# Performance work log

Measured on AMD Instinct MI355X. Metric: run time of the kernel, lower is better.

The kernel has to match this reference:

```python
import jax, jax.numpy as jnp
import numpy as np

N_NODES = 100000
N_EDGES = 1600000
IN_FEATS = 256
HEADS = 4
OUT_FEATS = 32


def setup_inputs() -> dict:
    key = jax.random.key(0)
    k1, k2, k3, k4, k5, k6 = jax.random.split(key, 6)
    feat = jax.random.normal(k1, (N_NODES, IN_FEATS), dtype=jnp.float32)
    fc_w = jax.random.normal(k2, (HEADS * OUT_FEATS, IN_FEATS), dtype=jnp.float32) * (1.0 / np.sqrt(IN_FEATS))
    attn_l = jax.random.normal(k3, (1, HEADS, OUT_FEATS), dtype=jnp.float32) * 0.1
    attn_r = jax.random.normal(k4, (1, HEADS, OUT_FEATS), dtype=jnp.float32) * 0.1
    src = jax.random.randint(k5, (N_EDGES,), 0, N_NODES, dtype=jnp.int32)
    dst = jax.random.randint(k6, (N_EDGES,), 0, N_NODES, dtype=jnp.int32)
    return {"feat": feat, "fc_w": fc_w, "attn_l": attn_l, "attn_r": attn_r, "src": src, "dst": dst}


def reference(feat, fc_w, attn_l, attn_r, src, dst):
    # feat: [N, F_in]; fc_w: [H*D, F_in]; attn_l/r: [1, H, D]; src/dst: [E]
    N = feat.shape[0]
    H, D = attn_l.shape[1], attn_l.shape[2]
    # linear projection (no bias), viewed as [N, H, D]
    ft = (feat @ fc_w.T).reshape(N, H, D)
    # per-node attention logits
    el = jnp.einsum('nhd,hd->nh', ft, attn_l[0])  # [N, H]
    er = jnp.einsum('nhd,hd->nh', ft, attn_r[0])  # [N, H]
    # per-edge score: leaky_relu(el[src] + er[dst])
    e = jax.nn.leaky_relu(el[src] + er[dst], negative_slope=0.2)  # [E, H]
    # edge softmax over incoming edges of each dst node (stable)
    emax = jax.ops.segment_max(e, dst, num_segments=N)  # [N, H]
    a = jnp.exp(e - emax[dst])  # [E, H]
    asum = jax.ops.segment_sum(a, dst, num_segments=N)  # [N, H]
    a = a / asum[dst]
    # attn_drop is a no-op in eval mode; weighted scatter-sum aggregation
    msg = ft[src] * a[:, :, None]  # [E, H, D]
    out = jax.ops.segment_sum(msg, dst, num_segments=N)  # [N, H, D]
    # final_layer=False, activation=None, norm=None -> flatten heads
    return out.reshape(N, H * D)
```

## Files before the change

kernel.cpp:

```cpp
#include <hip/hip_runtime.h>
#include <hip/hip_bf16.h>
#include <float.h>

#define IN_F 256
#define HD   128
#define NH   4

typedef __bf16 bf16x8 __attribute__((ext_vector_type(8)));
typedef __bf16 bf16x2 __attribute__((ext_vector_type(2)));
typedef float  f32x4  __attribute__((ext_vector_type(4)));

__device__ __forceinline__ bf16x8 cvt8(const float4 a, const float4 b) {
    bf16x8 r;
    r[0] = (__bf16)a.x; r[1] = (__bf16)a.y; r[2] = (__bf16)a.z; r[3] = (__bf16)a.w;
    r[4] = (__bf16)b.x; r[5] = (__bf16)b.y; r[6] = (__bf16)b.z; r[7] = (__bf16)b.w;
    return r;
}

__global__ __launch_bounds__(256) void wprep_k(const float* __restrict__ w,
                                               __bf16* __restrict__ wfrag) {
    const int idx = blockIdx.x * 256 + threadIdx.x;
    const int lane = idx & 63;
    const int ct = (idx >> 6) & 7;
    const int ks = idx >> 9;
    const float* p = w + (size_t)(ct * 16 + (lane & 15)) * IN_F + ks * 32 + (lane >> 4) * 8;
    const float4 v0 = *(const float4*)p;
    const float4 v1 = *(const float4*)(p + 4);
    *(bf16x8*)&wfrag[(size_t)idx * 8] = cvt8(v0, v1);
}

__global__ __launch_bounds__(256) void gemm_ft_fused(const float* __restrict__ feat,
                                                     const __bf16* __restrict__ wfrag,
                                                     const float* __restrict__ attn_l,
                                                     const float* __restrict__ attn_r,
                                                     __bf16* __restrict__ ft,
                                                     float* __restrict__ el,
                                                     float* __restrict__ er, int N) {
    const int t = threadIdx.x;
    const int wv = t >> 6;
    const int lane = t & 63;
    const int il = lane & 15;
    const int fk = (lane >> 4) * 8;
    const int rbase = blockIdx.x * 128 + wv * 32;

    f32x4 acc[2][8];
#pragma unroll
    for (int mt = 0; mt < 2; ++mt)
#pragma unroll
        for (int ct = 0; ct < 8; ++ct) acc[mt][ct] = {0.f, 0.f, 0.f, 0.f};

    const int r0 = rbase + il;
    const int r1 = rbase + 16 + il;

    for (int ks = 0; ks < 8; ++ks) {
        bf16x8 af0, af1;
        {
            if (r0 < N) {
                const float* p = feat + (size_t)r0 * IN_F + ks * 32 + fk;
                af0 = cvt8(*(const float4*)p, *(const float4*)(p + 4));
            } else {
#pragma unroll
                for (int i = 0; i < 8; ++i) af0[i] = (__bf16)0.f;
            }
            if (r1 < N) {
                const float* p = feat + (size_t)r1 * IN_F + ks * 32 + fk;
                af1 = cvt8(*(const float4*)p, *(const float4*)(p + 4));
            } else {
#pragma unroll
                for (int i = 0; i < 8; ++i) af1[i] = (__bf16)0.f;
            }
        }
        const bf16x8* bp = (const bf16x8*)&wfrag[(size_t)(ks * 8) * 512 + lane * 8];
#pragma unroll
        for (int ct = 0; ct < 8; ++ct) {
            const bf16x8 bfrag = bp[ct * 64];
            acc[0][ct] = __builtin_amdgcn_mfma_f32_16x16x32_bf16(af0, bfrag, acc[0][ct], 0, 0, 0);
            acc[1][ct] = __builtin_amdgcn_mfma_f32_16x16x32_bf16(af1, bfrag, acc[1][ct], 0, 0, 0);
        }
    }

    float AL[8], AR[8];
#pragma unroll
    for (int ct = 0; ct < 8; ++ct) {
        AL[ct] = attn_l[ct * 16 + il];
        AR[ct] = attn_r[ct * 16 + il];
    }

    const int rquad = (lane >> 4) * 4;
#pragma unroll
    for (int mt = 0; mt < 2; ++mt) {
#pragma unroll
        for (int reg = 0; reg < 4; ++reg) {
            const int row = rbase + mt * 16 + rquad + reg;
#pragma unroll
            for (int ct = 0; ct < 8; ++ct)
                if (row < N) ft[(size_t)row * HD + ct * 16 + il] = (__bf16)acc[mt][ct][reg];
            float pl[NH], pr[NH];
#pragma unroll
            for (int h = 0; h < NH; ++h) {
                const float v0 = acc[mt][2 * h][reg], v1 = acc[mt][2 * h + 1][reg];
                pl[h] = v0 * AL[2 * h] + v1 * AL[2 * h + 1];
                pr[h] = v0 * AR[2 * h] + v1 * AR[2 * h + 1];
            }
#pragma unroll
            for (int s = 1; s < 16; s <<= 1) {
#pragma unroll
                for (int h = 0; h < NH; ++h) {
                    pl[h] += __shfl_xor(pl[h], s);
                    pr[h] += __shfl_xor(pr[h], s);
                }
            }
            if (il < 8 && row < N) {
                const int h = il & 3;
                const float v = (h == 0) ? ((il < 4) ? pl[0] : pr[0])
                              : (h == 1) ? ((il < 4) ? pl[1] : pr[1])
                              : (h == 2) ? ((il < 4) ? pl[2] : pr[2])
                                         : ((il < 4) ? pl[3] : pr[3]);
                ((il < 4) ? el : er)[(size_t)row * NH + h] = v;
            }
        }
    }
}

__global__ __launch_bounds__(256) void deg_rank_k(const int* __restrict__ dst,
                                                  int* __restrict__ deg,
                                                  int* __restrict__ rank, int E) {
    const int i = blockIdx.x * 256 + threadIdx.x;
    if (i < E) rank[i] = atomicAdd(&deg[dst[i]], 1);
}

__global__ __launch_bounds__(1024) void scan1_k(const int* __restrict__ deg,
                                                int* __restrict__ off,
                                                int* __restrict__ bsum, int N) {
    __shared__ int wsum[16];
    const int t = threadIdx.x;
    const int lane = t & 63;
    const int wid = t >> 6;
    const int g = blockIdx.x * 1024 + t;
    const int x = (g < N) ? deg[g] : 0;
    int v = x;
#pragma unroll
    for (int s = 1; s < 64; s <<= 1) {
        const int u = __shfl_up(v, s);
        if (lane >= s) v += u;
    }
    if (lane == 63) wsum[wid] = v;
    __syncthreads();
    if (t < 16) {
        int wv_ = wsum[t];
#pragma unroll
        for (int s = 1; s < 16; s <<= 1) {
            const int u = __shfl_up(wv_, s);
            if (t >= s) wv_ += u;
        }
        wsum[t] = wv_;
    }
    __syncthreads();
    const int woff = wid ? wsum[wid - 1] : 0;
    if (g < N) off[g] = woff + v - x;
    if (t == 1023) bsum[blockIdx.x] = wsum[15];
}

__global__ __launch_bounds__(128) void scan2_k(const int* __restrict__ bsum,
                                               int* __restrict__ boff, int nb) {
    __shared__ int lds[128];
    const int t = threadIdx.x;
    const int x = (t < nb) ? bsum[t] : 0;
    lds[t] = x;
    __syncthreads();
    int v = x;
    for (int s = 1; s < 128; s <<= 1) {
        const int add = (t >= s) ? lds[t - s] : 0;
        __syncthreads();
        v += add;
        lds[t] = v;
        __syncthreads();
    }
    boff[t] = v - x;
}

__global__ __launch_bounds__(256) void scatter_k(const int* __restrict__ src,
                                                 const int* __restrict__ dst,
                                                 const int* __restrict__ off,
                                                 const int* __restrict__ boff,
                                                 const int* __restrict__ rank,
                                                 int* __restrict__ ssrc, int E) {
    const int i = blockIdx.x * 256 + threadIdx.x;
    if (i < E) {
        const int d = dst[i];
        const int p = off[d] + boff[d >> 10] + rank[i];
        ssrc[p] = src[i];
    }
}

__global__ __launch_bounds__(64) void aggregate_k(const __bf16* __restrict__ ft,
                                                  const float* __restrict__ el,
                                                  const float* __restrict__ er,
                                                  const int* __restrict__ deg,
                                                  const int* __restrict__ off,
                                                  const int* __restrict__ boff,
                                                  const int* __restrict__ ssrc,
                                                  float* __restrict__ out, int N) {
    const int n = blockIdx.x;
    const int lane = threadIdx.x;
    const int il = lane & 15;
    const int q  = lane >> 4;
    const int h  = il >> 2;
    float4* outp = (float4*)(out + (size_t)n * HD);
    const int dn = deg[n];
    if (dn == 0) {
        if (q < 2) outp[il * 2 + q] = make_float4(0.f, 0.f, 0.f, 0.f);
        return;
    }
    const int start = off[n] + boff[n >> 10];
    const float4 er4 = *(const float4*)(er + (size_t)n * NH);

    __shared__ float a_lds[64 * NH];
    __shared__ int   s_lds[64];
    float4 ssum = make_float4(0.f, 0.f, 0.f, 0.f);
    float acc[8];
#pragma unroll
    for (int i = 0; i < 8; ++i) acc[i] = 0.f;

    for (int c0 = 0; c0 < dn; c0 += 64) {
        const int j = c0 + lane;
        float4 a = make_float4(0.f, 0.f, 0.f, 0.f);
        int sv = 0;
        if (j < dn) {
            sv = ssrc[start + j];
            float4 e = *(const float4*)(el + (size_t)sv * NH);
            e.x += er4.x; e.y += er4.y; e.z += er4.z; e.w += er4.w;
            e.x = e.x >= 0.f ? e.x : 0.2f * e.x;
            e.y = e.y >= 0.f ? e.y : 0.2f * e.y;
            e.z = e.z >= 0.f ? e.z : 0.2f * e.z;
            e.w = e.w >= 0.f ? e.w : 0.2f * e.w;
            a.x = __expf(e.x); a.y = __expf(e.y);
            a.z = __expf(e.z); a.w = __expf(e.w);
            ssum.x += a.x; ssum.y += a.y; ssum.z += a.z; ssum.w += a.w;
        }
        s_lds[lane] = sv;
        *(float4*)(a_lds + lane * NH) = a;
        __syncthreads();
        const int cnt16 = (min(64, dn - c0) + 15) & ~15;
        for (int j2 = 0; j2 < cnt16; j2 += 16) {
            const int e0 = j2 + q, e1 = j2 + 4 + q, e2 = j2 + 8 + q, e3 = j2 + 12 + q;
            const int sv0 = s_lds[e0], sv1 = s_lds[e1], sv2 = s_lds[e2], sv3 = s_lds[e3];
            const float a0 = a_lds[e0 * NH + h], a1 = a_lds[e1 * NH + h];
            const float a2 = a_lds[e2 * NH + h], a3 = a_lds[e3 * NH + h];
            const bf16x8 f0 = *(const bf16x8*)(ft + (size_t)sv0 * HD + il * 8);
            const bf16x8 f1 = *(const bf16x8*)(ft + (size_t)sv1 * HD + il * 8);
            const bf16x8 f2 = *(const bf16x8*)(ft + (size_t)sv2 * HD + il * 8);
            const bf16x8 f3 = *(const bf16x8*)(ft + (size_t)sv3 * HD + il * 8);
#pragma unroll
            for (int k = 0; k < 8; ++k) acc[k] = fmaf(a0, (float)f0[k], acc[k]);
#pragma unroll
            for (int k = 0; k < 8; ++k) acc[k] = fmaf(a1, (float)f1[k], acc[k]);
#pragma unroll
            for (int k = 0; k < 8; ++k) acc[k] = fmaf(a2, (float)f2[k], acc[k]);
#pragma unroll
            for (int k = 0; k < 8; ++k) acc[k] = fmaf(a3, (float)f3[k], acc[k]);
        }
        __syncthreads();
    }
#pragma unroll
    for (int s = 1; s < 64; s <<= 1) {
        ssum.x += __shfl_xor(ssum.x, s);
        ssum.y += __shfl_xor(ssum.y, s);
        ssum.z += __shfl_xor(ssum.z, s);
        ssum.w += __shfl_xor(ssum.w, s);
    }
#pragma unroll
    for (int k = 0; k < 8; ++k) {
        acc[k] += __shfl_xor(acc[k], 16);
        acc[k] += __shfl_xor(acc[k], 32);
    }
    const float sumh = (h == 0) ? ssum.x : (h == 1) ? ssum.y : (h == 2) ? ssum.z : ssum.w;
    const float inv = 1.f / sumh;
    if (q < 2) {
        const int b = q * 4;
        outp[il * 2 + q] = make_float4(acc[b] * inv, acc[b + 1] * inv,
                                       acc[b + 2] * inv, acc[b + 3] * inv);
    }
}

extern "C" void kernel_launch(void* const* d_in, const int* in_sizes, int n_in,
                              void* d_out, int out_size, void* d_ws, size_t ws_size,
                              hipStream_t stream) {
    const float* feat   = (const float*)d_in[0];
    const float* fc_w   = (const float*)d_in[1];
    const float* attn_l = (const float*)d_in[2];
    const float* attn_r = (const float*)d_in[3];
    const int*   src    = (const int*)d_in[4];
    const int*   dst    = (const int*)d_in[5];
    const int N = in_sizes[0] / IN_F;
    const int E = in_sizes[4];
    float* out = (float*)d_out;

    char* wp = (char*)d_ws;
    __bf16* ft = (__bf16*)wp;    wp += (size_t)N * HD * 2;
    __bf16* wfrag = (__bf16*)wp; wp += 32768 * 2;
    float* el  = (float*)wp; wp += (size_t)N * NH * 4;
    float* er  = (float*)wp; wp += (size_t)N * NH * 4;
    int* deg   = (int*)wp;   wp += (size_t)N * 4;
    int* off   = (int*)wp;   wp += (size_t)N * 4;
    int* bsum  = (int*)wp;   wp += 1024;
    int* boff  = (int*)wp;   wp += 1024;
    int* rank  = (int*)wp;   wp += (size_t)E * 4;
    int* ssrc  = (int*)wp;   wp += (size_t)E * 4;

    hipMemsetAsync(deg, 0, (size_t)N * 4, stream);

    wprep_k<<<dim3(16), dim3(256), 0, stream>>>(fc_w, wfrag);
    gemm_ft_fused<<<dim3((N + 127) / 128), dim3(256), 0, stream>>>(
        feat, wfrag, attn_l, attn_r, ft, el, er, N);
    deg_rank_k<<<dim3((E + 255) / 256), dim3(256), 0, stream>>>(dst, deg, rank, E);
    const int nblk = (N + 1023) >> 10;
    scan1_k<<<dim3(nblk), dim3(1024), 0, stream>>>(deg, off, bsum, N);
    scan2_k<<<dim3(1), dim3(128), 0, stream>>>(bsum, boff, nblk);
    scatter_k<<<dim3((E + 255) / 256), dim3(256), 0, stream>>>(src, dst, off, boff, rank, ssrc, E);
    aggregate_k<<<dim3(N), dim3(64), 0, stream>>>(ft, el, er, deg, off, boff, ssrc, out, N);
}
```

Measured before the change: 394.7 us.

## Fold attention vectors into GEMM weights and use atomic-cursor CSR scatter

Precomputes W^T·attn_l and W^T·attn_r as a ninth MFMA column tile, so el/er come straight out of the GEMM instead of a cross-lane shuffle reduction. The CSR build drops the per-edge rank array: the histogram kernel only counts, a new combine kernel writes per-node cursors, and the scatter claims slots with atomicAdd on those cursors. Edge loads in the histogram and scatter kernels are vectorised to four edges per thread. This removes the shuffle epilogue and the rank array's E-sized write and read, at the cost of one extra kernel launch, an extra GEMM column tile, a nondeterministic neighbour order within each node, and el/er now taken from bf16-rounded folded weights.

Result: slower. 471.1 us (+19.3%).

```diff
diff --git a/kernel.cpp b/kernel.cpp
--- a/kernel.cpp
+++ b/kernel.cpp
@@ -5,9 +5,9 @@
 #define IN_F 256
 #define HD   128
 #define NH   4
+#define NCT  9
 
 typedef __bf16 bf16x8 __attribute__((ext_vector_type(8)));
-typedef __bf16 bf16x2 __attribute__((ext_vector_type(2)));
 typedef float  f32x4  __attribute__((ext_vector_type(4)));
 
 __device__ __forceinline__ bf16x8 cvt8(const float4 a, const float4 b) {
@@ -18,21 +18,39 @@
 }
 
 __global__ __launch_bounds__(256) void wprep_k(const float* __restrict__ w,
+                                               const float* __restrict__ attn_l,
+                                               const float* __restrict__ attn_r,
                                                __bf16* __restrict__ wfrag) {
     const int idx = blockIdx.x * 256 + threadIdx.x;
+    if (idx >= 8 * NCT * 64) return;
     const int lane = idx & 63;
-    const int ct = (idx >> 6) & 7;
-    const int ks = idx >> 9;
-    const float* p = w + (size_t)(ct * 16 + (lane & 15)) * IN_F + ks * 32 + (lane >> 4) * 8;
-    const float4 v0 = *(const float4*)p;
-    const float4 v1 = *(const float4*)(p + 4);
-    *(bf16x8*)&wfrag[(size_t)idx * 8] = cvt8(v0, v1);
+    const int ct = (idx >> 6) % NCT;
+    const int ks = idx / (NCT * 64);
+    const int il = lane & 15;
+    const int kk = ks * 32 + (lane >> 4) * 8;
+    bf16x8 r;
+    if (ct < 8) {
+        const float* p = w + (size_t)(ct * 16 + il) * IN_F + kk;
+        r = cvt8(*(const float4*)p, *(const float4*)(p + 4));
+    } else if (il < 8) {
+        const int h = il & 3;
+        const float* av = (il < 4) ? attn_l : attn_r;
+#pragma unroll
+        for (int j = 0; j < 8; ++j) {
+            float s = 0.f;
+            for (int d = 0; d < 32; ++d)
+                s += w[(size_t)(h * 32 + d) * IN_F + kk + j] * av[h * 32 + d];
+            r[j] = (__bf16)s;
+        }
+    } else {
+#pragma unroll
+        for (int j = 0; j < 8; ++j) r[j] = (__bf16)0.f;
+    }
+    *(bf16x8*)&wfrag[(size_t)idx * 8] = r;
 }
 
 __global__ __launch_bounds__(256) void gemm_ft_fused(const float* __restrict__ feat,
                                                      const __bf16* __restrict__ wfrag,
-                                                     const float* __restrict__ attn_l,
-                                                     const float* __restrict__ attn_r,
                                                      __bf16* __restrict__ ft,
                                                      float* __restrict__ el,
                                                      float* __restrict__ er, int N) {
@@ -43,90 +61,69 @@
     const int fk = (lane >> 4) * 8;
     const int rbase = blockIdx.x * 128 + wv * 32;
 
-    f32x4 acc[2][8];
+    f32x4 acc[2][NCT];
 #pragma unroll
     for (int mt = 0; mt < 2; ++mt)
 #pragma unroll
-        for (int ct = 0; ct < 8; ++ct) acc[mt][ct] = {0.f, 0.f, 0.f, 0.f};
+        for (int ct = 0; ct < NCT; ++ct) acc[mt][ct] = {0.f, 0.f, 0.f, 0.f};
 
     const int r0 = rbase + il;
     const int r1 = rbase + 16 + il;
 
     for (int ks = 0; ks < 8; ++ks) {
         bf16x8 af0, af1;
-        {
-            if (r0 < N) {
-                const float* p = feat + (size_t)r0 * IN_F + ks * 32 + fk;
-                af0 = cvt8(*(const float4*)p, *(const float4*)(p + 4));
-            } else {
-#pragma unroll
-                for (int i = 0; i < 8; ++i) af0[i] = (__bf16)0.f;
-            }
-            if (r1 < N) {
-                const float* p = feat + (size_t)r1 * IN_F + ks * 32 + fk;
-                af1 = cvt8(*(const float4*)p, *(const float4*)(p + 4));
-            } else {
-#pragma unroll
-                for (int i = 0; i < 8; ++i) af1[i] = (__bf16)0.f;
-            }
-        }
-        const bf16x8* bp = (const bf16x8*)&wfrag[(size_t)(ks * 8) * 512 + lane * 8];
-#pragma unroll
-        for (int ct = 0; ct < 8; ++ct) {
+        if (r0 < N) {
+            const float* p = feat + (size_t)r0 * IN_F + ks * 32 + fk;
+            af0 = cvt8(*(const float4*)p, *(const float4*)(p + 4));
+        } else {
+#pragma unroll
+            for (int i = 0; i < 8; ++i) af0[i] = (__bf16)0.f;
+        }
+        if (r1 < N) {
+            const float* p = feat + (size_t)r1 * IN_F + ks * 32 + fk;
+            af1 = cvt8(*(const float4*)p, *(const float4*)(p + 4));
+        } else {
+#pragma unroll
+            for (int i = 0; i < 8; ++i) af1[i] = (__bf16)0.f;
+        }
+        const bf16x8* bp = (const bf16x8*)&wfrag[(size_t)(ks * NCT) * 512 + lane * 8];
+#pragma unroll
+        for (int ct = 0; ct < NCT; ++ct) {
             const bf16x8 bfrag = bp[ct * 64];
             acc[0][ct] = __builtin_amdgcn_mfma_f32_16x16x32_bf16(af0, bfrag, acc[0][ct], 0, 0, 0);
             acc[1][ct] = __builtin_amdgcn_mfma_f32_16x16x32_bf16(af1, bfrag, acc[1][ct], 0, 0, 0);
         }
     }
 
-    float AL[8], AR[8];
-#pragma unroll
-    for (int ct = 0; ct < 8; ++ct) {
-        AL[ct] = attn_l[ct * 16 + il];
-        AR[ct] = attn_r[ct * 16 + il];
-    }
-
     const int rquad = (lane >> 4) * 4;
 #pragma unroll
     for (int mt = 0; mt < 2; ++mt) {
 #pragma unroll
         for (int reg = 0; reg < 4; ++reg) {
             const int row = rbase + mt * 16 + rquad + reg;
-#pragma unroll
-            for (int ct = 0; ct < 8; ++ct)
-                if (row < N) ft[(size_t)row * HD + ct * 16 + il] = (__bf16)acc[mt][ct][reg];
-            float pl[NH], pr[NH];
-#pragma unroll
-            for (int h = 0; h < NH; ++h) {
-                const float v0 = acc[mt][2 * h][reg], v1 = acc[mt][2 * h + 1][reg];
-                pl[h] = v0 * AL[2 * h] + v1 * AL[2 * h + 1];
-                pr[h] = v0 * AR[2 * h] + v1 * AR[2 * h + 1];
+            if (row < N) {
+#pragma unroll
+                for (int ct = 0; ct < 8; ++ct)
+                    ft[(size_t)row * HD + ct * 16 + il] = (__bf16)acc[mt][ct][reg];
+                if (il < 4)      el[(size_t)row * NH + il]       = acc[mt][8][reg];
+                else if (il < 8) er[(size_t)row * NH + (il - 4)] = acc[mt][8][reg];
             }
-#pragma unroll
-            for (int s = 1; s < 16; s <<= 1) {
-#pragma unroll
-                for (int h = 0; h < NH; ++h) {
-                    pl[h] += __shfl_xor(pl[h], s);
-                    pr[h] += __shfl_xor(pr[h], s);
-                }
-            }
-            if (il < 8 && row < N) {
-                const int h = il & 3;
-                const float v = (h == 0) ? ((il < 4) ? pl[0] : pr[0])
-                              : (h == 1) ? ((il < 4) ? pl[1] : pr[1])
-                              : (h == 2) ? ((il < 4) ? pl[2] : pr[2])
-                                         : ((il < 4) ? pl[3] : pr[3]);
-                ((il < 4) ? el : er)[(size_t)row * NH + h] = v;
-            }
-        }
-    }
-}
-
-__global__ __launch_bounds__(256) void deg_rank_k(const int* __restrict__ dst,
-                                                  int* __restrict__ deg,
-                                                  int* __restrict__ rank, int E) {
-    const int i = blockIdx.x * 256 + threadIdx.x;
-    if (i < E) rank[i] = atomicAdd(&deg[dst[i]], 1);
+        }
+    }
+}
+
+__global__ __launch_bounds__(256) void histo_k(const int* __restrict__ dst,
+                                               int* __restrict__ deg, int E) {
+    const int i0 = (blockIdx.x * 256 + threadIdx.x) * 4;
+    if (i0 + 3 < E) {
+        const int4 d4 = *(const int4*)(dst + i0);
+        atomicAdd(&deg[d4.x], 1);
+        atomicAdd(&deg[d4.y], 1);
+        atomicAdd(&deg[d4.z], 1);
+        atomicAdd(&deg[d4.w], 1);
+    } else {
+        for (int i = i0; i < E; ++i) atomicAdd(&deg[dst[i]], 1);
+    }
 }
 
 __global__ __launch_bounds__(1024) void scan1_k(const int* __restrict__ deg,
@@ -179,17 +176,28 @@
     boff[t] = v - x;
 }
 
+__global__ __launch_bounds__(256) void combine_k(const int* __restrict__ off,
+                                                 const int* __restrict__ boff,
+                                                 int* __restrict__ cursor, int N) {
+    const int g = blockIdx.x * 256 + threadIdx.x;
+    if (g < N) cursor[g] = off[g] + boff[g >> 10];
+}
+
 __global__ __launch_bounds__(256) void scatter_k(const int* __restrict__ src,
                                                  const int* __restrict__ dst,
-                                                 const int* __restrict__ off,
-                                                 const int* __restrict__ boff,
-                                                 const int* __restrict__ rank,
+                                                 int* __restrict__ cursor,
                                                  int* __restrict__ ssrc, int E) {
-    const int i = blockIdx.x * 256 + threadIdx.x;
-    if (i < E) {
-        const int d = dst[i];
-        const int p = off[d] + boff[d >> 10] + rank[i];
-        ssrc[p] = src[i];
+    const int i0 = (blockIdx.x * 256 + threadIdx.x) * 4;
+    if (i0 + 3 < E) {
+        const int4 s4 = *(const int4*)(src + i0);
+        const int4 d4 = *(const int4*)(dst + i0);
+        ssrc[atomicAdd(&cursor[d4.x], 1)] = s4.x;
+        ssrc[atomicAdd(&cursor[d4.y], 1)] = s4.y;
+        ssrc[atomicAdd(&cursor[d4.z], 1)] = s4.z;
+        ssrc[atomicAdd(&cursor[d4.w], 1)] = s4.w;
+    } else {
+        for (int i = i0; i < E; ++i)
+            ssrc[atomicAdd(&cursor[dst[i]], 1)] = src[i];
     }
 }
 
@@ -197,8 +205,7 @@
                                                   const float* __restrict__ el,
                                                   const float* __restrict__ er,
                                                   const int* __restrict__ deg,
-                                                  const int* __restrict__ off,
-                                                  const int* __restrict__ boff,
+                                                  const int* __restrict__ cursor,
                                                   const int* __restrict__ ssrc,
                                                   float* __restrict__ out, int N) {
     const int n = blockIdx.x;
@@ -212,7 +219,7 @@
         if (q < 2) outp[il * 2 + q] = make_float4(0.f, 0.f, 0.f, 0.f);
         return;
     }
-    const int start = off[n] + boff[n >> 10];
+    const int start = cursor[n] - dn;
     const float4 er4 = *(const float4*)(er + (size_t)n * NH);
 
     __shared__ float a_lds[64 * NH];
@@ -298,25 +305,26 @@
 
     char* wp = (char*)d_ws;
     __bf16* ft = (__bf16*)wp;    wp += (size_t)N * HD * 2;
-    __bf16* wfrag = (__bf16*)wp; wp += 32768 * 2;
+    __bf16* wfrag = (__bf16*)wp; wp += 8 * NCT * 512 * 2;
     float* el  = (float*)wp; wp += (size_t)N * NH * 4;
     float* er  = (float*)wp; wp += (size_t)N * NH * 4;
-    int* deg   = (int*)wp;   wp += (size_t)N * 4;
-    int* off   = (int*)wp;   wp += (size_t)N * 4;
-    int* bsum  = (int*)wp;   wp += 1024;
-    int* boff  = (int*)wp;   wp += 1024;
-    int* rank  = (int*)wp;   wp += (size_t)E * 4;
-    int* ssrc  = (int*)wp;   wp += (size_t)E * 4;
+    int* deg    = (int*)wp;  wp += (size_t)N * 4;
+    int* off    = (int*)wp;  wp += (size_t)N * 4;
+    int* cursor = (int*)wp;  wp += (size_t)N * 4;
+    int* bsum   = (int*)wp;  wp += 1024;
+    int* boff   = (int*)wp;  wp += 1024;
+    int* ssrc   = (int*)wp;  wp += (size_t)E * 4;
 
     hipMemsetAsync(deg, 0, (size_t)N * 4, stream);
 
-    wprep_k<<<dim3(16), dim3(256), 0, stream>>>(fc_w, wfrag);
+    wprep_k<<<dim3(18), dim3(256), 0, stream>>>(fc_w, attn_l, attn_r, wfrag);
     gemm_ft_fused<<<dim3((N + 127) / 128), dim3(256), 0, stream>>>(
-        feat, wfrag, attn_l, attn_r, ft, el, er, N);
-    deg_rank_k<<<dim3((E + 255) / 256), dim3(256), 0, stream>>>(dst, deg, rank, E);
+        feat, wfrag, ft, el, er, N);
+    histo_k<<<dim3((E / 4 + 255) / 256), dim3(256), 0, stream>>>(dst, deg, E);
     const int nblk = (N + 1023) >> 10;
     scan1_k<<<dim3(nblk), dim3(1024), 0, stream>>>(deg, off, bsum, N);
     scan2_k<<<dim3(1), dim3(128), 0, stream>>>(bsum, boff, nblk);
-    scatter_k<<<dim3((E + 255) / 256), dim3(256), 0, stream>>>(src, dst, off, boff, rank, ssrc, E);
-    aggregate_k<<<dim3(N), dim3(64), 0, stream>>>(ft, el, er, deg, off, boff, ssrc, out, N);
-}
+    combine_k<<<dim3((N + 255) / 256), dim3(256), 0, stream>>>(off, boff, cursor, N);
+    scatter_k<<<dim3((E / 4 + 255) / 256), dim3(256), 0, stream>>>(src, dst, cursor, ssrc, E);
+    aggregate_k<<<dim3(N), dim3(64), 0, stream>>>(ft, el, er, deg, cursor, ssrc, out, N);
+}
```
